# Kernel tuning notes

Measured on AMD Instinct MI355X. Metric: run time of the kernel, lower is better.

## Reference

```python
import jax, jax.numpy as jnp
import numpy as np

NUM_EXPERTS = 8
TOP_K = 2

def setup_inputs() -> dict:
    key = jax.random.key(0)
    k1, k2, k3, k4 = jax.random.split(key, 4)
    B, L, D, F, E = 2, 2048, 1024, 2048, NUM_EXPERTS
    layer_input = jax.random.normal(k1, (B, L, D), dtype=jnp.float32)
    router_w = jax.random.normal(k2, (E, D), dtype=jnp.float32) * 0.02
    # input_linear.weight.transpose(2,1) in torch -> [E, D, 2F] layout here
    w1 = jax.random.normal(k3, (E, D, 2 * F), dtype=jnp.float32) * 0.02
    # output_linear.weight.transpose(2,1) -> [E, F, D]
    w2 = jax.random.normal(k4, (E, F, D), dtype=jnp.float32) * 0.02
    return {"layer_input": layer_input, "router_w": router_w, "w1": w1, "w2": w2}


def reference(layer_input, router_w, w1, w2):
    B, L, D = layer_input.shape
    E = router_w.shape[0]
    x = layer_input.reshape(-1, D)                              # [N, D]
    router_logits = x @ router_w.T                              # [N, E]
    probs = jax.nn.softmax(router_logits.astype(jnp.float32), axis=-1)
    routing_weights, selected = jax.lax.top_k(probs, TOP_K)     # [N, K]
    routing_weights = routing_weights / routing_weights.sum(-1, keepdims=True)
    routing_weights = routing_weights.astype(x.dtype)

    out = jnp.zeros_like(x)
    # Fixed small loop over experts; same math as sorted grouped-GEMM + scatter-combine.
    for e in range(E):
        gate_e = jnp.sum(jnp.where(selected == e, routing_weights, 0.0), axis=-1)  # [N]
        gh = x @ w1[e]                                          # [N, 2F]
        g, h = jnp.split(gh, 2, axis=-1)
        y = (jax.nn.silu(g) * h) @ w2[e]                        # [N, D]
        out = out + gate_e[:, None] * y
    return out.reshape(B, L, D)
```

## Files before the change

kernel.cpp:

```cpp
#include <hip/hip_runtime.h>
#include <stdint.h>

typedef unsigned short u16;
typedef __attribute__((ext_vector_type(8))) short short8;
typedef __attribute__((ext_vector_type(4))) float floatx4;

#define NTOK 4096
#define DDIM 1024
#define FDIM 2048
#define NEXP 8

__device__ __forceinline__ u16 f2bf(float f) {
    union { float f; uint32_t u; } v; v.f = f;
    uint32_t r = v.u + 0x7fff + ((v.u >> 16) & 1);
    return (u16)(r >> 16);
}
__device__ __forceinline__ uint32_t pk2(float a, float b) {
    return (uint32_t)f2bf(a) | ((uint32_t)f2bf(b) << 16);
}
__device__ __forceinline__ void gl_lds16(const u16* g, u16* l) {
    __builtin_amdgcn_global_load_lds(
        (const __attribute__((address_space(1))) uint32_t*)g,
        (__attribute__((address_space(3))) uint32_t*)l, 16, 0, 0);
}

__global__ __launch_bounds__(256)
void router_kernel(const float* __restrict__ x, const float* __restrict__ rw,
                   int* __restrict__ topk_e, float* __restrict__ topk_w,
                   u16* __restrict__ xb) {
    const int lane = threadIdx.x & 63;
    const int wv = threadIdx.x >> 6;
    const int tok = blockIdx.x * 4 + wv;
    const float* xr = x + (size_t)tok * DDIM;
    u16* xo = xb + (size_t)tok * DDIM;
    float acc[8];
#pragma unroll
    for (int e = 0; e < 8; ++e) acc[e] = 0.f;
#pragma unroll
    for (int it = 0; it < 4; ++it) {
        int d0 = (it * 64 + lane) * 4;
        float4 xv = *(const float4*)(xr + d0);
        uint2 o = { pk2(xv.x, xv.y), pk2(xv.z, xv.w) };
        *(uint2*)(xo + d0) = o;
#pragma unroll
        for (int e = 0; e < 8; ++e) {
            float4 wv4 = *(const float4*)(rw + (size_t)e * DDIM + d0);
            acc[e] += xv.x * wv4.x + xv.y * wv4.y + xv.z * wv4.z + xv.w * wv4.w;
        }
    }
#pragma unroll
    for (int s = 32; s > 0; s >>= 1)
#pragma unroll
        for (int e = 0; e < 8; ++e) acc[e] += __shfl_down(acc[e], s);
    if (lane == 0) {
        int e0 = 0;
#pragma unroll
        for (int e = 1; e < 8; ++e) if (acc[e] > acc[e0]) e0 = e;
        int e1 = (e0 == 0) ? 1 : 0;
#pragma unroll
        for (int e = 0; e < 8; ++e) if (e != e0 && acc[e] > acc[e1]) e1 = e;
        float w0 = 1.f / (1.f + __expf(acc[e1] - acc[e0]));
        topk_e[tok * 2 + 0] = e0;
        topk_e[tok * 2 + 1] = e1;
        topk_w[tok * 2 + 0] = w0;
        topk_w[tok * 2 + 1] = 1.f - w0;
    }
}

__global__ __launch_bounds__(256)
void prefix_kernel(const int* __restrict__ topk_e, int* __restrict__ counts,
                   int* __restrict__ offs, int* __restrict__ cursors) {
    __shared__ int h[NEXP];
    const int t = threadIdx.x;
    if (t < NEXP) h[t] = 0;
    __syncthreads();
    int c[NEXP];
#pragma unroll
    for (int j = 0; j < NEXP; ++j) c[j] = 0;
    const int4* te4 = (const int4*)topk_e;
#pragma unroll
    for (int it = 0; it < 8; ++it) {
        int4 v = te4[it * 256 + t];
#pragma unroll
        for (int j = 0; j < NEXP; ++j)
            c[j] += (v.x == j) + (v.y == j) + (v.z == j) + (v.w == j);
    }
#pragma unroll
    for (int j = 0; j < NEXP; ++j)
        if (c[j]) atomicAdd(&h[j], c[j]);
    __syncthreads();
    if (t == 0) {
        int s = 0;
        for (int e = 0; e < NEXP; ++e) {
            counts[e] = h[e];
            offs[e] = s;
            s += h[e];
        }
        offs[NEXP] = s;
    }
    if (t < NEXP) cursors[t] = 0;
}

__global__ __launch_bounds__(256)
void build_rows(const int* __restrict__ topk_e, const int* __restrict__ offs,
                int* __restrict__ cursors, int* __restrict__ row_tok,
                float* __restrict__ gate_row, const float* __restrict__ topk_w) {
    __shared__ int lcnt[NEXP];
    __shared__ int lbase[NEXP];
    const int t = threadIdx.x;
    if (t < NEXP) lcnt[t] = 0;
    __syncthreads();
    const int tok = blockIdx.x * 256 + t;
    const int e0 = topk_e[tok * 2 + 0];
    const int e1 = topk_e[tok * 2 + 1];
    const int s0 = atomicAdd(&lcnt[e0], 1);
    const int s1 = atomicAdd(&lcnt[e1], 1);
    __syncthreads();
    if (t < NEXP) lbase[t] = lcnt[t] ? atomicAdd(&cursors[t], lcnt[t]) : 0;
    __syncthreads();
    int r0 = offs[e0] + lbase[e0] + s0;
    row_tok[r0] = tok;
    gate_row[r0] = topk_w[tok * 2 + 0];
    int r1 = offs[e1] + lbase[e1] + s1;
    row_tok[r1] = tok;
    gate_row[r1] = topk_w[tok * 2 + 1];
}

__global__ __launch_bounds__(256)
void transpose_f32_bf16(const float* __restrict__ src, u16* __restrict__ dst,
                        int R, int C) {
    __shared__ float tile[64][65];
    size_t eo = (size_t)blockIdx.z * R * C;
    const float* S = src + eo;
    u16* D = dst + eo;
    int r0 = blockIdx.y * 64, c0 = blockIdx.x * 64;
    int t = threadIdx.x;
    int rr = t >> 4;
    int cc = (t & 15) * 4;
#pragma unroll
    for (int it = 0; it < 4; ++it) {
        int r = rr + it * 16;
        float4 v = *(const float4*)(S + (size_t)(r0 + r) * C + (c0 + cc));
        tile[cc + 0][r] = v.x; tile[cc + 1][r] = v.y;
        tile[cc + 2][r] = v.z; tile[cc + 3][r] = v.w;
    }
    __syncthreads();
#pragma unroll
    for (int it = 0; it < 2; ++it) {
        int u = it * 256 + t;
        int c = u >> 3;
        int rv = (u & 7) * 8;
        uint4 o;
        o.x = pk2(tile[c][rv + 0], tile[c][rv + 1]);
        o.y = pk2(tile[c][rv + 2], tile[c][rv + 3]);
        o.z = pk2(tile[c][rv + 4], tile[c][rv + 5]);
        o.w = pk2(tile[c][rv + 6], tile[c][rv + 7]);
        *(uint4*)(D + (size_t)(c0 + c) * R + (r0 + rv)) = o;
    }
}

__global__ __launch_bounds__(256, 2)
void gemm1_fast(const u16* __restrict__ xb, const u16* __restrict__ w1b,
                u16* __restrict__ act, const int* __restrict__ row_tok,
                const int* __restrict__ counts, const int* __restrict__ offs) {
    const int bid = blockIdx.x;
    const int e = bid & 7;
    const int cnt = counts[e];
    const int nmb = (cnt + 127) >> 7;
    const int j = bid >> 3;
    if (j >= nmb * 32) return;
    const int m0 = (j % nmb) * 128;
    const int n0 = (j / nmb) * 64;
    const int off = offs[e];

    __shared__ __align__(16) u16 As[2 * 128 * 32];
    __shared__ __align__(16) u16 Bs[2 * 128 * 32];

    const int t = threadIdx.x;
    const int lane = t & 63;
    const int wv = t >> 6;
    const int quad = lane >> 4;
    const int rr = lane & 15;
    const int wm = (wv & 1) * 64;
    const int wn = (wv >> 1) * 32;

    const int scol = (lane & 3) * 8;
    const u16* arA[2];
    const u16* arB[2];
#pragma unroll
    for (int i = 0; i < 2; ++i) {
        int m = wv * 32 + i * 16 + ((lane >> 2) & 15);
        int r = m0 + m; if (r >= cnt) r = cnt - 1;
        arA[i] = xb + (size_t)row_tok[off + r] * DDIM + scol;
        int br = wv * 32 + i * 16 + ((lane >> 2) & 15);
        size_t brow = (br < 64) ? ((size_t)e * 4096 + n0 + br)
                                : ((size_t)e * 4096 + 2048 + n0 + (br - 64));
        arB[i] = w1b + brow * DDIM + scol;
    }
    u16* dstA[2][2];
    u16* dstB[2][2];
#pragma unroll
    for (int s = 0; s < 2; ++s)
#pragma unroll
        for (int i = 0; i < 2; ++i) {
            dstA[s][i] = &As[(s * 128 + wv * 32 + i * 16) * 32];
            dstB[s][i] = &Bs[(s * 128 + wv * 32 + i * 16) * 32];
        }

    floatx4 accg[4][2] = {};
    floatx4 acch[4][2] = {};

    for (int k0 = 0; k0 < DDIM; k0 += 64) {
        __syncthreads();
#pragma unroll
        for (int s = 0; s < 2; ++s)
#pragma unroll
            for (int i = 0; i < 2; ++i) {
                gl_lds16(arA[i] + k0 + s * 32, dstA[s][i]);
                gl_lds16(arB[i] + k0 + s * 32, dstB[s][i]);
            }
        __syncthreads();

#pragma unroll
        for (int s = 0; s < 2; ++s) {
            short8 af[4], bg[2], bh[2];
#pragma unroll
            for (int mt = 0; mt < 4; ++mt)
                af[mt] = *(const short8*)&As[(s * 128 + wm + mt * 16 + rr) * 32 + quad * 8];
#pragma unroll
            for (int nt = 0; nt < 2; ++nt) {
                bg[nt] = *(const short8*)&Bs[(s * 128 + wn + nt * 16 + rr) * 32 + quad * 8];
                bh[nt] = *(const short8*)&Bs[(s * 128 + 64 + wn + nt * 16 + rr) * 32 + quad * 8];
            }
#pragma unroll
            for (int mt = 0; mt < 4; ++mt)
#pragma unroll
                for (int nt = 0; nt < 2; ++nt) {
                    accg[mt][nt] = __builtin_amdgcn_mfma_f32_16x16x32_bf16(af[mt], bg[nt], accg[mt][nt], 0, 0, 0);
                    acch[mt][nt] = __builtin_amdgcn_mfma_f32_16x16x32_bf16(af[mt], bh[nt], acch[mt][nt], 0, 0, 0);
                }
        }
    }
#pragma unroll
    for (int mt = 0; mt < 4; ++mt)
#pragma unroll
        for (int nt = 0; nt < 2; ++nt)
#pragma unroll
            for (int rg = 0; rg < 4; ++rg) {
                int gm = m0 + wm + mt * 16 + quad * 4 + rg;
                if (gm < cnt) {
                    float g = accg[mt][nt][rg];
                    float h = acch[mt][nt][rg];
                    float s = g / (1.f + __expf(-g));
                    act[(size_t)(off + gm) * FDIM + (n0 + wn + nt * 16 + rr)] = f2bf(s * h);
                }
            }
}

__global__ __launch_bounds__(256, 2)
void gemm2_fast(const u16* __restrict__ act, const u16* __restrict__ w2b,
                float* __restrict__ out, const int* __restrict__ row_tok,
                const float* __restrict__ gate_row, const int* __restrict__ counts,
                const int* __restrict__ offs) {
    const int bid = blockIdx.x;
    const int e = bid & 7;
    const int cnt = counts[e];
    const int nmb = (cnt + 127) >> 7;
    const int j = bid >> 3;
    if (j >= nmb * 8) return;
    const int m0 = (j % nmb) * 128;
    const int n0 = (j / nmb) * 128;
    const int off = offs[e];

    __shared__ __align__(16) u16 As[2 * 128 * 32];
    __shared__ __align__(16) u16 Bs[2 * 128 * 32];

    const int t = threadIdx.x;
    const int lane = t & 63;
    const int wv = t >> 6;
    const int quad = lane >> 4;
    const int rr = lane & 15;
    const int wm = (wv & 1) * 64;
    const int wn = (wv >> 1) * 64;

    const int scol = (lane & 3) * 8;
    const u16* arA[2];
    const u16* arB[2];
#pragma unroll
    for (int i = 0; i < 2; ++i) {
        int m = wv * 32 + i * 16 + ((lane >> 2) & 15);
        int r = m0 + m; if (r >= cnt) r = cnt - 1;
        arA[i] = act + (size_t)(off + r) * FDIM + scol;
        arB[i] = w2b + ((size_t)e * 1024 + n0 + m) * FDIM + scol;
    }
    u16* dstA[2][2];
    u16* dstB[2][2];
#pragma unroll
    for (int s = 0; s < 2; ++s)
#pragma unroll
        for (int i = 0; i < 2; ++i) {
            dstA[s][i] = &As[(s * 128 + wv * 32 + i * 16) * 32];
            dstB[s][i] = &Bs[(s * 128 + wv * 32 + i * 16) * 32];
        }

    floatx4 acc[4][4] = {};

    for (int k0 = 0; k0 < FDIM; k0 += 64) {
        __syncthreads();
#pragma unroll
        for (int s = 0; s < 2; ++s)
#pragma unroll
            for (int i = 0; i < 2; ++i) {
                gl_lds16(arA[i] + k0 + s * 32, dstA[s][i]);
                gl_lds16(arB[i] + k0 + s * 32, dstB[s][i]);
            }
        __syncthreads();

#pragma unroll
        for (int s = 0; s < 2; ++s) {
            short8 af[4], bf[4];
#pragma unroll
            for (int mt = 0; mt < 4; ++mt)
                af[mt] = *(const short8*)&As[(s * 128 + wm + mt * 16 + rr) * 32 + quad * 8];
#pragma unroll
            for (int nt = 0; nt < 4; ++nt)
                bf[nt] = *(const short8*)&Bs[(s * 128 + wn + nt * 16 + rr) * 32 + quad * 8];
#pragma unroll
            for (int mt = 0; mt < 4; ++mt)
#pragma unroll
                for (int nt = 0; nt < 4; ++nt)
                    acc[mt][nt] = __builtin_amdgcn_mfma_f32_16x16x32_bf16(af[mt], bf[nt], acc[mt][nt], 0, 0, 0);
        }
    }
#pragma unroll
    for (int mt = 0; mt < 4; ++mt)
#pragma unroll
        for (int rg = 0; rg < 4; ++rg) {
            int gm = m0 + wm + mt * 16 + quad * 4 + rg;
            if (gm < cnt) {
                int gr = off + gm;
                float gate = gate_row[gr];
                float* orow = out + (size_t)row_tok[gr] * DDIM + n0 + wn;
#pragma unroll
                for (int nt = 0; nt < 4; ++nt)
                    atomicAdd(&orow[nt * 16 + rr], gate * acc[mt][nt][rg]);
            }
        }
}

extern "C" void kernel_launch(void* const* d_in, const int* in_sizes, int n_in,
                              void* d_out, int out_size, void* d_ws, size_t ws_size,
                              hipStream_t stream) {
    const float* x  = (const float*)d_in[0];
    const float* rw = (const float*)d_in[1];
    const float* w1 = (const float*)d_in[2];
    const float* w2 = (const float*)d_in[3];
    float* out = (float*)d_out;

    char* ws = (char*)d_ws;
    const size_t MB = 1ull << 20;
    int*   counts   = (int*)(ws);
    int*   cursors  = (int*)(ws + 64);
    int*   offs     = (int*)(ws + 128);
    int*   topk_e   = (int*)(ws + 2048);
    float* topk_w   = (float*)(ws + 2048 + 32768);
    int*   row_tok  = (int*)(ws + 2048 + 65536);
    float* gate_row = (float*)(ws + 2048 + 98304);
    u16*   act      = (u16*)(ws + 1 * MB);
    u16*   xb       = (u16*)(ws + 33 * MB);
    u16*   w1b      = (u16*)(ws + 41 * MB);
    u16*   w2b      = (u16*)(ws + 41 * MB);

    hipMemsetAsync(out, 0, (size_t)out_size * 4, stream);
    router_kernel<<<dim3(NTOK / 4), 256, 0, stream>>>(x, rw, topk_e, topk_w, xb);
    prefix_kernel<<<1, 256, 0, stream>>>(topk_e, counts, offs, cursors);
    build_rows<<<dim3(NTOK / 256), 256, 0, stream>>>(topk_e, offs, cursors, row_tok, gate_row, topk_w);
    transpose_f32_bf16<<<dim3(4096 / 64, 1024 / 64, NEXP), 256, 0, stream>>>(w1, w1b, 1024, 4096);
    gemm1_fast<<<dim3(8192), 256, 0, stream>>>(xb, w1b, act, row_tok, counts, offs);
    transpose_f32_bf16<<<dim3(1024 / 64, 2048 / 64, NEXP), 256, 0, stream>>>(w2, w2b, 2048, 1024);
    gemm2_fast<<<dim3(2048), 256, 0, stream>>>(act, w2b, out, row_tok, gate_row, counts, offs);
    (void)in_sizes; (void)n_in; (void)ws_size;
}
```

Measured before the change: 442.3 us.

## Double-buffer LDS loads with vmcnt waits to overlap global loads and MFMA

Both expert GEMM kernels now use a two-buffer software pipeline in place of the load-all-then-sync loop. While MFMAs run on one 32-wide K slice, the next slice is already being fetched into the other LDS buffer via global_load_lds. Synchronisation uses explicit s_waitcnt vmcnt/lgkmcnt and raw s_barrier rather than __syncthreads. The aim is to hide global memory latency behind compute, at the cost of relying on hand-counted waitcnt values being correct.

```diff
diff --git a/kernel.cpp b/kernel.cpp
--- a/kernel.cpp
+++ b/kernel.cpp
@@ -23,6 +23,12 @@
         (const __attribute__((address_space(1))) uint32_t*)g,
         (__attribute__((address_space(3))) uint32_t*)l, 16, 0, 0);
 }
+
+#define WAITV4 asm volatile("s_waitcnt vmcnt(4)" ::: "memory")
+#define WAITV0 asm volatile("s_waitcnt vmcnt(0)" ::: "memory")
+#define LGKM0  asm volatile("s_waitcnt lgkmcnt(0)" ::: "memory")
+#define BAR    __builtin_amdgcn_s_barrier()
+#define CFENCE asm volatile("" ::: "memory")
 
 __global__ __launch_bounds__(256)
 void router_kernel(const float* __restrict__ x, const float* __restrict__ rw,
@@ -192,55 +198,56 @@
         int m = wv * 32 + i * 16 + ((lane >> 2) & 15);
         int r = m0 + m; if (r >= cnt) r = cnt - 1;
         arA[i] = xb + (size_t)row_tok[off + r] * DDIM + scol;
-        int br = wv * 32 + i * 16 + ((lane >> 2) & 15);
-        size_t brow = (br < 64) ? ((size_t)e * 4096 + n0 + br)
-                                : ((size_t)e * 4096 + 2048 + n0 + (br - 64));
+        size_t brow = (m < 64) ? ((size_t)e * 4096 + n0 + m)
+                               : ((size_t)e * 4096 + 2048 + n0 + (m - 64));
         arB[i] = w1b + brow * DDIM + scol;
     }
-    u16* dstA[2][2];
-    u16* dstB[2][2];
-#pragma unroll
-    for (int s = 0; s < 2; ++s)
-#pragma unroll
-        for (int i = 0; i < 2; ++i) {
-            dstA[s][i] = &As[(s * 128 + wv * 32 + i * 16) * 32];
-            dstB[s][i] = &Bs[(s * 128 + wv * 32 + i * 16) * 32];
-        }
+    u16* dA0 = &As[(wv * 32) * 32];
+    u16* dA1 = &As[(wv * 32 + 16) * 32];
+    u16* dB0 = &Bs[(wv * 32) * 32];
+    u16* dB1 = &Bs[(wv * 32 + 16) * 32];
 
     floatx4 accg[4][2] = {};
     floatx4 acch[4][2] = {};
 
-    for (int k0 = 0; k0 < DDIM; k0 += 64) {
-        __syncthreads();
-#pragma unroll
-        for (int s = 0; s < 2; ++s)
-#pragma unroll
-            for (int i = 0; i < 2; ++i) {
-                gl_lds16(arA[i] + k0 + s * 32, dstA[s][i]);
-                gl_lds16(arB[i] + k0 + s * 32, dstB[s][i]);
-            }
-        __syncthreads();
-
-#pragma unroll
-        for (int s = 0; s < 2; ++s) {
-            short8 af[4], bg[2], bh[2];
-#pragma unroll
-            for (int mt = 0; mt < 4; ++mt)
-                af[mt] = *(const short8*)&As[(s * 128 + wm + mt * 16 + rr) * 32 + quad * 8];
-#pragma unroll
-            for (int nt = 0; nt < 2; ++nt) {
-                bg[nt] = *(const short8*)&Bs[(s * 128 + wn + nt * 16 + rr) * 32 + quad * 8];
-                bh[nt] = *(const short8*)&Bs[(s * 128 + 64 + wn + nt * 16 + rr) * 32 + quad * 8];
-            }
-#pragma unroll
-            for (int mt = 0; mt < 4; ++mt)
-#pragma unroll
-                for (int nt = 0; nt < 2; ++nt) {
-                    accg[mt][nt] = __builtin_amdgcn_mfma_f32_16x16x32_bf16(af[mt], bg[nt], accg[mt][nt], 0, 0, 0);
-                    acch[mt][nt] = __builtin_amdgcn_mfma_f32_16x16x32_bf16(af[mt], bh[nt], acch[mt][nt], 0, 0, 0);
-                }
-        }
-    }
+#define G1_STAGE(b, ko)                                    \
+    { gl_lds16(arA[0] + (ko), dA0 + (b) * 4096);           \
+      gl_lds16(arA[1] + (ko), dA1 + (b) * 4096);           \
+      gl_lds16(arB[0] + (ko), dB0 + (b) * 4096);           \
+      gl_lds16(arB[1] + (ko), dB1 + (b) * 4096); }
+
+#define G1_COMPUTE(b)                                                                   \
+    { short8 af[4], bg[2], bh[2];                                                       \
+      _Pragma("unroll") for (int mt = 0; mt < 4; ++mt)                                  \
+          af[mt] = *(const short8*)&As[(b) * 4096 + (wm + mt * 16 + rr) * 32 + quad * 8];\
+      _Pragma("unroll") for (int nt = 0; nt < 2; ++nt) {                                \
+          bg[nt] = *(const short8*)&Bs[(b) * 4096 + (wn + nt * 16 + rr) * 32 + quad * 8];\
+          bh[nt] = *(const short8*)&Bs[(b) * 4096 + (64 + wn + nt * 16 + rr) * 32 + quad * 8]; } \
+      _Pragma("unroll") for (int mt = 0; mt < 4; ++mt)                                  \
+          _Pragma("unroll") for (int nt = 0; nt < 2; ++nt) {                            \
+              accg[mt][nt] = __builtin_amdgcn_mfma_f32_16x16x32_bf16(af[mt], bg[nt], accg[mt][nt], 0, 0, 0); \
+              acch[mt][nt] = __builtin_amdgcn_mfma_f32_16x16x32_bf16(af[mt], bh[nt], acch[mt][nt], 0, 0, 0); } }
+
+    G1_STAGE(0, 0);
+    for (int p = 0; p < 15; ++p) {
+        G1_STAGE(1, (2 * p + 1) * 32);
+        WAITV4; BAR; CFENCE;
+        G1_COMPUTE(0);
+        LGKM0; BAR; CFENCE;
+        G1_STAGE(0, (2 * p + 2) * 32);
+        WAITV4; BAR; CFENCE;
+        G1_COMPUTE(1);
+        LGKM0; BAR; CFENCE;
+    }
+    G1_STAGE(1, 31 * 32);
+    WAITV4; BAR; CFENCE;
+    G1_COMPUTE(0);
+    CFENCE;
+    WAITV0; BAR; CFENCE;
+    G1_COMPUTE(1);
+#undef G1_STAGE
+#undef G1_COMPUTE
+
 #pragma unroll
     for (int mt = 0; mt < 4; ++mt)
 #pragma unroll
@@ -293,45 +300,49 @@
         arA[i] = act + (size_t)(off + r) * FDIM + scol;
         arB[i] = w2b + ((size_t)e * 1024 + n0 + m) * FDIM + scol;
     }
-    u16* dstA[2][2];
-    u16* dstB[2][2];
-#pragma unroll
-    for (int s = 0; s < 2; ++s)
-#pragma unroll
-        for (int i = 0; i < 2; ++i) {
-            dstA[s][i] = &As[(s * 128 + wv * 32 + i * 16) * 32];
-            dstB[s][i] = &Bs[(s * 128 + wv * 32 + i * 16) * 32];
-        }
+    u16* dA0 = &As[(wv * 32) * 32];
+    u16* dA1 = &As[(wv * 32 + 16) * 32];
+    u16* dB0 = &Bs[(wv * 32) * 32];
+    u16* dB1 = &Bs[(wv * 32 + 16) * 32];
 
     floatx4 acc[4][4] = {};
 
-    for (int k0 = 0; k0 < FDIM; k0 += 64) {
-        __syncthreads();
-#pragma unroll
-        for (int s = 0; s < 2; ++s)
-#pragma unroll
-            for (int i = 0; i < 2; ++i) {
-                gl_lds16(arA[i] + k0 + s * 32, dstA[s][i]);
-                gl_lds16(arB[i] + k0 + s * 32, dstB[s][i]);
-            }
-        __syncthreads();
-
-#pragma unroll
-        for (int s = 0; s < 2; ++s) {
-            short8 af[4], bf[4];
-#pragma unroll
-            for (int mt = 0; mt < 4; ++mt)
-                af[mt] = *(const short8*)&As[(s * 128 + wm + mt * 16 + rr) * 32 + quad * 8];
-#pragma unroll
-            for (int nt = 0; nt < 4; ++nt)
-                bf[nt] = *(const short8*)&Bs[(s * 128 + wn + nt * 16 + rr) * 32 + quad * 8];
-#pragma unroll
-            for (int mt = 0; mt < 4; ++mt)
-#pragma unroll
-                for (int nt = 0; nt < 4; ++nt)
-                    acc[mt][nt] = __builtin_amdgcn_mfma_f32_16x16x32_bf16(af[mt], bf[nt], acc[mt][nt], 0, 0, 0);
-        }
-    }
+#define G2_STAGE(b, ko)                                    \
+    { gl_lds16(arA[0] + (ko), dA0 + (b) * 4096);           \
+      gl_lds16(arA[1] + (ko), dA1 + (b) * 4096);           \
+      gl_lds16(arB[0] + (ko), dB0 + (b) * 4096);           \
+      gl_lds16(arB[1] + (ko), dB1 + (b) * 4096); }
+
+#define G2_COMPUTE(b)                                                                   \
+    { short8 af[4], bf[4];                                                              \
+      _Pragma("unroll") for (int mt = 0; mt < 4; ++mt)                                  \
+          af[mt] = *(const short8*)&As[(b) * 4096 + (wm + mt * 16 + rr) * 32 + quad * 8];\
+      _Pragma("unroll") for (int nt = 0; nt < 4; ++nt)                                  \
+          bf[nt] = *(const short8*)&Bs[(b) * 4096 + (wn + nt * 16 + rr) * 32 + quad * 8];\
+      _Pragma("unroll") for (int mt = 0; mt < 4; ++mt)                                  \
+          _Pragma("unroll") for (int nt = 0; nt < 4; ++nt)                              \
+              acc[mt][nt] = __builtin_amdgcn_mfma_f32_16x16x32_bf16(af[mt], bf[nt], acc[mt][nt], 0, 0, 0); }
+
+    G2_STAGE(0, 0);
+    for (int p = 0; p < 31; ++p) {
+        G2_STAGE(1, (2 * p + 1) * 32);
+        WAITV4; BAR; CFENCE;
+        G2_COMPUTE(0);
+        LGKM0; BAR; CFENCE;
+        G2_STAGE(0, (2 * p + 2) * 32);
+        WAITV4; BAR; CFENCE;
+        G2_COMPUTE(1);
+        LGKM0; BAR; CFENCE;
+    }
+    G2_STAGE(1, 63 * 32);
+    WAITV4; BAR; CFENCE;
+    G2_COMPUTE(0);
+    CFENCE;
+    WAITV0; BAR; CFENCE;
+    G2_COMPUTE(1);
+#undef G2_STAGE
+#undef G2_COMPUTE
+
 #pragma unroll
     for (int mt = 0; mt < 4; ++mt)
 #pragma unroll
```

Result: slower. 456.4 us (+3.2%).
